# Kernel tuning notes

Measured on AMD Instinct MI355X. Metric: run time of the kernel, lower is better.

## Reference

```python
import jax, jax.numpy as jnp
import numpy as np

Q_LORA, KV_LORA = 1536, 512
NUM_HEADS, HEAD_DIM = 4, 64
B, QL, KL = 2, 4096, 4096


def setup_inputs() -> dict:
    key = jax.random.key(0)
    k1, k2, k3, k4 = jax.random.split(key, 4)
    q_compressed = jax.random.normal(k1, (B, QL, Q_LORA), dtype=jnp.float32)
    kv_compressed = jax.random.normal(k2, (B, KL, KV_LORA), dtype=jnp.float32)
    # additive causal mask: 0 on/below diagonal, -inf-like above
    causal_mask = jnp.where(
        jnp.arange(QL)[:, None] >= jnp.arange(KL)[None, :], 0.0, -1e9
    ).astype(jnp.float32)
    # learned params (Linear weights stored torch-style as [out, in])
    Wq = 0.01 * jax.random.normal(k3, (NUM_HEADS * HEAD_DIM, Q_LORA), dtype=jnp.float32)
    Wk = 0.01 * jax.random.normal(k4, (NUM_HEADS * HEAD_DIM, KV_LORA), dtype=jnp.float32)
    head_weights = jnp.ones((NUM_HEADS,), dtype=jnp.float32)
    return {
        "q_compressed": q_compressed,
        "kv_compressed": kv_compressed,
        "causal_mask": causal_mask,
        "Wq": Wq,
        "Wk": Wk,
        "head_weights": head_weights,
    }


def reference(q_compressed, kv_compressed, causal_mask, Wq, Wk, head_weights):
    b, ql, _ = q_compressed.shape
    kl = kv_compressed.shape[1]
    # projections: x @ W.T, then split heads
    q_idx = (q_compressed @ Wq.T).reshape(b, ql, NUM_HEADS, HEAD_DIM)  # [b,q,h,d]
    k_idx = (kv_compressed @ Wk.T).reshape(b, kl, NUM_HEADS, HEAD_DIM)  # [b,k,h,d]
    scores = jnp.einsum("bqhd,bkhd->bhqk", q_idx, k_idx)
    scores = jax.nn.relu(scores)
    # head-weighted sum over heads
    index_scores = jnp.einsum("bhqk,h->bqk", scores, head_weights)
    index_scores = index_scores + causal_mask[None, :, :]
    return index_scores
```

## Files before the change

kernel.cpp:

```cpp
#include <hip/hip_runtime.h>
#include <hip/hip_bf16.h>
#include <stdint.h>

typedef __attribute__((ext_vector_type(8))) short bhalf8;
typedef __attribute__((ext_vector_type(4))) float f32x4;
typedef __attribute__((ext_vector_type(4))) unsigned us4;

#define B_ 2
#define QL_ 4096
#define KL_ 4096
#define ND_ 256
#define QLORA_ 1536
#define KVLORA_ 512

__device__ __forceinline__ unsigned pack2(float lo, float hi) {
    union { float f; unsigned u; } a, b; a.f = lo; b.f = hi;
    return __builtin_amdgcn_perm(b.u, a.u, 0x07060302u);
}

__global__ __launch_bounds__(256, 4) void prep_kernel(
    const float* __restrict__ qc, const float* __restrict__ kvc,
    const float* __restrict__ Wq, const float* __restrict__ Wk,
    unsigned short* __restrict__ qidx, unsigned short* __restrict__ kidx)
{
    const int bid = blockIdx.x;
    const int tid = threadIdx.x;

    const float* A; const float* W; unsigned short* C; int K; int pb;
    if (bid < 512) { A = qc;  W = Wq; C = qidx; K = QLORA_;  pb = bid; }
    else           { A = kvc; W = Wk; C = kidx; K = KVLORA_; pb = bid - 512; }

    __shared__ unsigned short sA[2][64][72];
    __shared__ unsigned short sW[2][64][72];

    const int lane = tid & 63;
    const int wid = tid >> 6;

    const int t2 = pb >> 3;
    const int nt = t2 & 3;
    const int mt = (pb & 7) + 8 * (t2 >> 2);
    const int m0 = mt * 64, n0 = nt * 64;

    const int wm = (wid >> 1) * 32;
    const int wn = (wid & 1) * 32;

    const int sr = tid >> 3;
    const int sc = (tid & 7) * 8;

    const float* Abase = A + (size_t)(m0 + sr) * K + sc;
    const float* Wbase = W + (size_t)(n0 + sr) * K + sc;
    const size_t row32 = (size_t)32 * K;

    f32x4 pa[4], pw[4], qa[4], qw[4];
    f32x4 acc[2][2] = {};
    const int nIter = K >> 6;

    auto ISSUE = [&](int kk, f32x4* ra, f32x4* rw) {
        #pragma unroll
        for (int p = 0; p < 2; ++p) {
            ra[2 * p]     = *reinterpret_cast<const f32x4*>(Abase + row32 * p + kk);
            ra[2 * p + 1] = *reinterpret_cast<const f32x4*>(Abase + row32 * p + kk + 4);
            rw[2 * p]     = *reinterpret_cast<const f32x4*>(Wbase + row32 * p + kk);
            rw[2 * p + 1] = *reinterpret_cast<const f32x4*>(Wbase + row32 * p + kk + 4);
        }
        __builtin_amdgcn_sched_barrier(0);
    };
    auto WRITE = [&](int buf, f32x4* ra, f32x4* rw) {
        #pragma unroll
        for (int p = 0; p < 2; ++p) {
            us4 va = { pack2(ra[2*p][0], ra[2*p][1]), pack2(ra[2*p][2], ra[2*p][3]),
                       pack2(ra[2*p+1][0], ra[2*p+1][1]), pack2(ra[2*p+1][2], ra[2*p+1][3]) };
            *reinterpret_cast<us4*>(&sA[buf][sr + 32 * p][sc]) = va;
            us4 vw = { pack2(rw[2*p][0], rw[2*p][1]), pack2(rw[2*p][2], rw[2*p][3]),
                       pack2(rw[2*p+1][0], rw[2*p+1][1]), pack2(rw[2*p+1][2], rw[2*p+1][3]) };
            *reinterpret_cast<us4*>(&sW[buf][sr + 32 * p][sc]) = vw;
        }
    };
    auto COMPUTE = [&](int buf) {
        #pragma unroll
        for (int ks = 0; ks < 2; ++ks) {
            const int cb = ks * 32 + (lane >> 4) * 8;
            bhalf8 a0 = *reinterpret_cast<const bhalf8*>(&sA[buf][wm + (lane & 15)][cb]);
            bhalf8 a1 = *reinterpret_cast<const bhalf8*>(&sA[buf][wm + 16 + (lane & 15)][cb]);
            bhalf8 b0 = *reinterpret_cast<const bhalf8*>(&sW[buf][wn + (lane & 15)][cb]);
            bhalf8 b1 = *reinterpret_cast<const bhalf8*>(&sW[buf][wn + 16 + (lane & 15)][cb]);
            acc[0][0] = __builtin_amdgcn_mfma_f32_16x16x32_bf16(a0, b0, acc[0][0], 0, 0, 0);
            acc[0][1] = __builtin_amdgcn_mfma_f32_16x16x32_bf16(a0, b1, acc[0][1], 0, 0, 0);
            acc[1][0] = __builtin_amdgcn_mfma_f32_16x16x32_bf16(a1, b0, acc[1][0], 0, 0, 0);
            acc[1][1] = __builtin_amdgcn_mfma_f32_16x16x32_bf16(a1, b1, acc[1][1], 0, 0, 0);
        }
    };

    ISSUE(0, pa, pw);
    WRITE(0, pa, pw);
    ISSUE(64, pa, pw);
    __syncthreads();

    for (int it = 0; it < nIter; it += 2) {
        if (it + 2 < nIter) ISSUE((it + 2) << 6, qa, qw);
        COMPUTE(0);
        if (it + 1 < nIter) WRITE(1, pa, pw);
        __syncthreads();
        if (it + 3 < nIter) ISSUE((it + 3) << 6, pa, pw);
        COMPUTE(1);
        if (it + 2 < nIter) WRITE(0, qa, qw);
        __syncthreads();
    }

    #pragma unroll
    for (int i = 0; i < 2; ++i) {
        #pragma unroll
        for (int j = 0; j < 2; ++j) {
            int n = n0 + wn + j * 16 + (lane & 15);
            #pragma unroll
            for (int r = 0; r < 4; ++r) {
                int m = m0 + wm + i * 16 + (lane >> 4) * 4 + r;
                union { float f; unsigned u; } x; x.f = acc[i][j][r];
                C[(size_t)m * ND_ + n] = (unsigned short)(x.u >> 16);
            }
        }
    }
}

__global__ __launch_bounds__(512, 2) void scores_kernel(
    const unsigned short* __restrict__ Qi,
    const unsigned short* __restrict__ Ki,
    const float* __restrict__ hw,
    float* __restrict__ out)
{
    const int bx = blockIdx.x;
    const int tid = threadIdx.x;

    if (bx >= 1056) {
        int t = bx - 1056;
        int b = (t >= 496) ? 1 : 0;
        t -= b * 496;
        int tk = (int)((1.0f + __builtin_sqrtf(8.0f * (float)t + 1.0f)) * 0.5f);
        while (tk * (tk - 1) / 2 > t) --tk;
        while (tk * (tk + 1) / 2 <= t) ++tk;
        int tq = t - tk * (tk - 1) / 2;
        float* outb = out + (size_t)b * QL_ * KL_ + (size_t)tq * 128 * KL_ + tk * 128;
        const f32x4 mval = {-1e9f, -1e9f, -1e9f, -1e9f};
        #pragma unroll
        for (int p = 0; p < 8; ++p) {
            int idx = p * 512 + tid;
            int r = idx >> 5;
            int c = (idx & 31) * 4;
            *reinterpret_cast<f32x4*>(&outb[(size_t)r * KL_ + c]) = mval;
        }
        return;
    }

    int g = (bx & 7) * 132 + (bx >> 3);
    int b = (g >= 528) ? 1 : 0;
    int t = g - b * 528;
    int tq = (int)((__builtin_sqrtf(8.0f * (float)t + 1.0f) - 1.0f) * 0.5f);
    while ((tq + 1) * (tq + 2) / 2 <= t) ++tq;
    while (tq * (tq + 1) / 2 > t) --tq;
    int tk = t - tq * (tq + 1) / 2;

    const int q0 = tq * 128, k0 = tk * 128;
    float* outb = out + (size_t)b * QL_ * KL_;

    __shared__ unsigned short sQ[2][128][72];
    __shared__ unsigned short sK[2][128][72];
    const int lane = tid & 63;
    const int wid = tid >> 6;
    const int wq = (wid >> 2) * 64;
    const int wk = (wid & 3) * 32;
    const int l15 = lane & 15;
    const int lh = lane >> 4;

    const int hr = tid >> 2;
    const int hc = (tid & 3) * 16;

    float whv[4];
    #pragma unroll
    for (int h = 0; h < 4; ++h) whv[h] = hw[h];

    f32x4 acc[4][2] = {};
    bhalf8 rq0, rq1, rk0, rk1;

    const unsigned short* Qb = Qi + (size_t)(b * QL_ + q0) * ND_;
    const unsigned short* Kb = Ki + (size_t)(b * KL_ + k0) * ND_;

    auto LOADH = [&](int h) {
        const size_t ro = (size_t)hr * ND_ + h * 64 + hc;
        rq0 = *reinterpret_cast<const bhalf8*>(&Qb[ro]);
        rq1 = *reinterpret_cast<const bhalf8*>(&Qb[ro + 8]);
        rk0 = *reinterpret_cast<const bhalf8*>(&Kb[ro]);
        rk1 = *reinterpret_cast<const bhalf8*>(&Kb[ro + 8]);
    };
    auto WRITEH = [&](int buf) {
        *reinterpret_cast<bhalf8*>(&sQ[buf][hr][hc])     = rq0;
        *reinterpret_cast<bhalf8*>(&sQ[buf][hr][hc + 8]) = rq1;
        *reinterpret_cast<bhalf8*>(&sK[buf][hr][hc])     = rk0;
        *reinterpret_cast<bhalf8*>(&sK[buf][hr][hc + 8]) = rk1;
    };
    auto COMPUTE_H = [&](int buf, int h) {
        f32x4 hacc[4][2] = {};
        #pragma unroll
        for (int ks = 0; ks < 2; ++ks) {
            const int cb = ks * 32 + lh * 8;
            bhalf8 kfr[2];
            #pragma unroll
            for (int j = 0; j < 2; ++j)
                kfr[j] = *reinterpret_cast<const bhalf8*>(&sK[buf][wk + j * 16 + l15][cb]);
            #pragma unroll
            for (int i = 0; i < 4; ++i) {
                bhalf8 qfr = *reinterpret_cast<const bhalf8*>(&sQ[buf][wq + i * 16 + l15][cb]);
                #pragma unroll
                for (int j = 0; j < 2; ++j)
                    hacc[i][j] = __builtin_amdgcn_mfma_f32_16x16x32_bf16(qfr, kfr[j], hacc[i][j], 0, 0, 0);
            }
        }
        const float wgt = whv[h];
        const f32x4 zero = {0.0f, 0.0f, 0.0f, 0.0f};
        #pragma unroll
        for (int i = 0; i < 4; ++i)
            #pragma unroll
            for (int j = 0; j < 2; ++j) {
                f32x4 m = __builtin_elementwise_max(hacc[i][j], zero);
                acc[i][j] += wgt * m;
            }
    };

    LOADH(0);
    WRITEH(0);
    __syncthreads();
    #pragma unroll
    for (int h = 0; h < 4; ++h) {
        if (h < 3) LOADH(h + 1);
        COMPUTE_H(h & 1, h);
        if (h < 3) {
            WRITEH((h + 1) & 1);
            __syncthreads();
        }
    }

    const int kcb = k0 + wk + l15;
    if (tq == tk) {
        #pragma unroll
        for (int i = 0; i < 4; ++i)
            #pragma unroll
            for (int r = 0; r < 4; ++r) {
                int q = q0 + wq + i * 16 + lh * 4 + r;
                #pragma unroll
                for (int j = 0; j < 2; ++j) {
                    int kc = kcb + j * 16;
                    outb[(size_t)q * KL_ + kc] = acc[i][j][r] + ((kc <= q) ? 0.0f : -1e9f);
                }
            }
    } else {
        #pragma unroll
        for (int i = 0; i < 4; ++i)
            #pragma unroll
            for (int r = 0; r < 4; ++r) {
                int q = q0 + wq + i * 16 + lh * 4 + r;
                #pragma unroll
                for (int j = 0; j < 2; ++j)
                    outb[(size_t)q * KL_ + kcb + j * 16] = acc[i][j][r];
            }
    }
}

extern "C" void kernel_launch(void* const* d_in, const int* in_sizes, int n_in,
                              void* d_out, int out_size, void* d_ws, size_t ws_size,
                              hipStream_t stream) {
    const float* qc  = (const float*)d_in[0];
    const float* kvc = (const float*)d_in[1];
    const float* Wq  = (const float*)d_in[3];
    const float* Wk  = (const float*)d_in[4];
    const float* hw  = (const float*)d_in[5];

    unsigned short* qidx = (unsigned short*)d_ws;
    unsigned short* kidx = qidx + (size_t)B_ * QL_ * ND_;

    prep_kernel<<<dim3(1024), 256, 0, stream>>>(qc, kvc, Wq, Wk, qidx, kidx);
    scores_kernel<<<dim3(1056 + 992), 512, 0, stream>>>(qidx, kidx, hw, (float*)d_out);
}
```

Before: 60.63 us.

## Use 4 waves with 64x64 per-wave tiles and single-buffered LDS in scores kernel

```diff
diff --git a/kernel.cpp b/kernel.cpp
--- a/kernel.cpp
+++ b/kernel.cpp
@@ -122,7 +122,7 @@
     }
 }
 
-__global__ __launch_bounds__(512, 2) void scores_kernel(
+__global__ __launch_bounds__(256, 3) void scores_kernel(
     const unsigned short* __restrict__ Qi,
     const unsigned short* __restrict__ Ki,
     const float* __restrict__ hw,
@@ -142,8 +142,8 @@
         float* outb = out + (size_t)b * QL_ * KL_ + (size_t)tq * 128 * KL_ + tk * 128;
         const f32x4 mval = {-1e9f, -1e9f, -1e9f, -1e9f};
         #pragma unroll
-        for (int p = 0; p < 8; ++p) {
-            int idx = p * 512 + tid;
+        for (int p = 0; p < 16; ++p) {
+            int idx = p * 256 + tid;
             int r = idx >> 5;
             int c = (idx & 31) * 4;
             *reinterpret_cast<f32x4*>(&outb[(size_t)r * KL_ + c]) = mval;
@@ -162,55 +162,57 @@
     const int q0 = tq * 128, k0 = tk * 128;
     float* outb = out + (size_t)b * QL_ * KL_;
 
-    __shared__ unsigned short sQ[2][128][72];
-    __shared__ unsigned short sK[2][128][72];
+    __shared__ unsigned short sQ[128][72];
+    __shared__ unsigned short sK[128][72];
     const int lane = tid & 63;
     const int wid = tid >> 6;
-    const int wq = (wid >> 2) * 64;
-    const int wk = (wid & 3) * 32;
+    const int wq = (wid >> 1) * 64;
+    const int wk = (wid & 1) * 64;
     const int l15 = lane & 15;
     const int lh = lane >> 4;
 
-    const int hr = tid >> 2;
-    const int hc = (tid & 3) * 16;
+    const int hr = tid >> 1;
+    const int hc = (tid & 1) * 32;
 
     float whv[4];
     #pragma unroll
     for (int h = 0; h < 4; ++h) whv[h] = hw[h];
 
-    f32x4 acc[4][2] = {};
-    bhalf8 rq0, rq1, rk0, rk1;
+    f32x4 acc[4][4] = {};
+    bhalf8 rq[4], rk[4];
 
     const unsigned short* Qb = Qi + (size_t)(b * QL_ + q0) * ND_;
     const unsigned short* Kb = Ki + (size_t)(b * KL_ + k0) * ND_;
 
     auto LOADH = [&](int h) {
         const size_t ro = (size_t)hr * ND_ + h * 64 + hc;
-        rq0 = *reinterpret_cast<const bhalf8*>(&Qb[ro]);
-        rq1 = *reinterpret_cast<const bhalf8*>(&Qb[ro + 8]);
-        rk0 = *reinterpret_cast<const bhalf8*>(&Kb[ro]);
-        rk1 = *reinterpret_cast<const bhalf8*>(&Kb[ro + 8]);
-    };
-    auto WRITEH = [&](int buf) {
-        *reinterpret_cast<bhalf8*>(&sQ[buf][hr][hc])     = rq0;
-        *reinterpret_cast<bhalf8*>(&sQ[buf][hr][hc + 8]) = rq1;
-        *reinterpret_cast<bhalf8*>(&sK[buf][hr][hc])     = rk0;
-        *reinterpret_cast<bhalf8*>(&sK[buf][hr][hc + 8]) = rk1;
-    };
-    auto COMPUTE_H = [&](int buf, int h) {
-        f32x4 hacc[4][2] = {};
+        #pragma unroll
+        for (int p = 0; p < 4; ++p) {
+            rq[p] = *reinterpret_cast<const bhalf8*>(&Qb[ro + p * 8]);
+            rk[p] = *reinterpret_cast<const bhalf8*>(&Kb[ro + p * 8]);
+        }
+    };
+    auto WRITEH = [&]() {
+        #pragma unroll
+        for (int p = 0; p < 4; ++p) {
+            *reinterpret_cast<bhalf8*>(&sQ[hr][hc + p * 8]) = rq[p];
+            *reinterpret_cast<bhalf8*>(&sK[hr][hc + p * 8]) = rk[p];
+        }
+    };
+    auto COMPUTE_H = [&](int h) {
+        f32x4 hacc[4][4] = {};
         #pragma unroll
         for (int ks = 0; ks < 2; ++ks) {
             const int cb = ks * 32 + lh * 8;
-            bhalf8 kfr[2];
-            #pragma unroll
-            for (int j = 0; j < 2; ++j)
-                kfr[j] = *reinterpret_cast<const bhalf8*>(&sK[buf][wk + j * 16 + l15][cb]);
+            bhalf8 kfr[4];
+            #pragma unroll
+            for (int j = 0; j < 4; ++j)
+                kfr[j] = *reinterpret_cast<const bhalf8*>(&sK[wk + j * 16 + l15][cb]);
             #pragma unroll
             for (int i = 0; i < 4; ++i) {
-                bhalf8 qfr = *reinterpret_cast<const bhalf8*>(&sQ[buf][wq + i * 16 + l15][cb]);
+                bhalf8 qfr = *reinterpret_cast<const bhalf8*>(&sQ[wq + i * 16 + l15][cb]);
                 #pragma unroll
-                for (int j = 0; j < 2; ++j)
+                for (int j = 0; j < 4; ++j)
                     hacc[i][j] = __builtin_amdgcn_mfma_f32_16x16x32_bf16(qfr, kfr[j], hacc[i][j], 0, 0, 0);
             }
         }
@@ -219,21 +221,22 @@
         #pragma unroll
         for (int i = 0; i < 4; ++i)
             #pragma unroll
-            for (int j = 0; j < 2; ++j) {
+            for (int j = 0; j < 4; ++j) {
                 f32x4 m = __builtin_elementwise_max(hacc[i][j], zero);
                 acc[i][j] += wgt * m;
             }
     };
 
     LOADH(0);
-    WRITEH(0);
+    WRITEH();
     __syncthreads();
     #pragma unroll
     for (int h = 0; h < 4; ++h) {
         if (h < 3) LOADH(h + 1);
-        COMPUTE_H(h & 1, h);
+        COMPUTE_H(h);
         if (h < 3) {
-            WRITEH((h + 1) & 1);
+            __syncthreads();
+            WRITEH();
             __syncthreads();
         }
     }
@@ -246,7 +249,7 @@
             for (int r = 0; r < 4; ++r) {
                 int q = q0 + wq + i * 16 + lh * 4 + r;
                 #pragma unroll
-                for (int j = 0; j < 2; ++j) {
+                for (int j = 0; j < 4; ++j) {
                     int kc = kcb + j * 16;
                     outb[(size_t)q * KL_ + kc] = acc[i][j][r] + ((kc <= q) ? 0.0f : -1e9f);
                 }
@@ -258,7 +261,7 @@
             for (int r = 0; r < 4; ++r) {
                 int q = q0 + wq + i * 16 + lh * 4 + r;
                 #pragma unroll
-                for (int j = 0; j < 2; ++j)
+                for (int j = 0; j < 4; ++j)
                     outb[(size_t)q * KL_ + kcb + j * 16] = acc[i][j][r];
             }
     }
@@ -277,5 +280,5 @@
     unsigned short* kidx = qidx + (size_t)B_ * QL_ * ND_;
 
     prep_kernel<<<dim3(1024), 256, 0, stream>>>(qc, kvc, Wq, Wk, qidx, kidx);
-    scores_kernel<<<dim3(1056 + 992), 512, 0, stream>>>(qidx, kidx, hw, (float*)d_out);
-}
+    scores_kernel<<<dim3(1056 + 992), 256, 0, stream>>>(qidx, kidx, hw, (float*)d_out);
+}
```

New measurement: 82.68 us. 1.36x slower.
